# Optimization experiments

Measured on AMD Instinct MI355X. Metric: run time of the kernel, lower is better.

## Reference

```python
import jax, jax.numpy as jnp
import numpy as np

EPS = 1e-5
K = 31  # large depthwise kernel
PAD = K // 2


def _bn(x, gamma, beta, mean, var):
    # x: [B, C, L]; params: [C]
    inv = gamma / jnp.sqrt(var + EPS)
    return x * inv[:, None] + (beta - mean * inv)[:, None]


def setup_inputs() -> dict:
    key = jax.random.key(0)
    ks = jax.random.split(key, 20)
    B, C, L = 32, 256, 4096
    H = 512  # hidden = C * expand_ratio(2)

    def bn_params(k, ch):
        k1, k2, k3, k4 = jax.random.split(k, 4)
        return (jax.random.normal(k1, (ch,)) * 0.1 + 1.0,   # gamma
                jax.random.normal(k2, (ch,)) * 0.1,          # beta
                jax.random.normal(k3, (ch,)) * 0.1,          # running mean
                jax.random.uniform(k4, (ch,)) * 0.5 + 0.5)   # running var

    g0, b0, m0, v0 = bn_params(ks[0], C)
    g1, b1, m1, v1 = bn_params(ks[1], H)
    g2, b2, m2, v2 = bn_params(ks[2], H)
    g3, b3, m3, v3 = bn_params(ks[3], C)

    return {
        "x": jax.random.normal(ks[4], (B, C, L), dtype=jnp.float32),
        "w_expand": jax.random.normal(ks[5], (H, C), dtype=jnp.float32) * (1.0 / np.sqrt(C)),
        "w_dw": jax.random.normal(ks[6], (H, 1, K), dtype=jnp.float32) * (1.0 / np.sqrt(K)),
        "w_project": jax.random.normal(ks[7], (C, H), dtype=jnp.float32) * (1.0 / np.sqrt(H)),
        "g0": g0, "b0": b0, "m0": m0, "v0": v0,
        "g1": g1, "b1": b1, "m1": m1, "v1": v1,
        "g2": g2, "b2": b2, "m2": m2, "v2": v2,
        "g3": g3, "b3": b3, "m3": m3, "v3": v3,
    }


def reference(x, w_expand, w_dw, w_project,
              g0, b0, m0, v0, g1, b1, m1, v1,
              g2, b2, m2, v2, g3, b3, m3, v3):
    shortcut = x
    # pre-norm BN
    h = _bn(x, g0, b0, m0, v0)
    # pw_expand: 1x1 conv (GEMM) + BN + ReLU -> [B, H, L]
    h = jnp.einsum("bcl,hc->bhl", h, w_expand)
    h = jax.nn.relu(_bn(h, g1, b1, m1, v1))
    # large-kernel depthwise conv + BN
    H = w_dw.shape[0]
    h = jax.lax.conv_general_dilated(
        h, w_dw, window_strides=(1,), padding=[(PAD, PAD)],
        dimension_numbers=("NCH", "OIH", "NCH"), feature_group_count=H)
    h = _bn(h, g2, b2, m2, v2)
    # activation then pw_project: 1x1 conv + BN -> [B, C, L]
    h = jax.nn.relu(h)
    h = jnp.einsum("bhl,ch->bcl", h, w_project)
    h = _bn(h, g3, b3, m3, v3)
    return shortcut + h  # drop_path=0 -> identity
```

## Files before the change

kernel.cpp:

```cpp
#include <hip/hip_runtime.h>
#include <hip/hip_bf16.h>

#define C_DIM 256
#define L_DIM 4096
#define H_DIM 512
#define KW    31
#define PADW  15

typedef unsigned short u16;
typedef unsigned int   u32;
typedef short bf16x8 __attribute__((ext_vector_type(8)));
typedef float f32x4  __attribute__((ext_vector_type(4)));

__device__ __forceinline__ u16 f2bf(float f) {
    u32 u = __float_as_uint(f);
    u32 r = (u + 0x7FFFu + ((u >> 16) & 1u)) >> 16;
    return (u16)r;
}
__device__ __forceinline__ float bf2f(u16 h) {
    return __uint_as_float(((u32)h) << 16);
}

typedef __attribute__((address_space(1))) const unsigned int gq_t;
typedef __attribute__((address_space(3))) unsigned int lq_t;
__device__ __forceinline__ void async16(void* lds, const void* g) {
    __builtin_amdgcn_global_load_lds((gq_t*)g, (lq_t*)lds, 16, 0, 0);
}

__global__ __launch_bounds__(256) void prep_kernel(
    const float* __restrict__ w_expand,
    const float* __restrict__ g0, const float* __restrict__ b0,
    const float* __restrict__ m0, const float* __restrict__ v0,
    const float* __restrict__ g1, const float* __restrict__ b1,
    const float* __restrict__ m1, const float* __restrict__ v1,
    const float* __restrict__ g2, const float* __restrict__ b2,
    const float* __restrict__ m2, const float* __restrict__ v2,
    const float* __restrict__ g3, const float* __restrict__ b3,
    const float* __restrict__ m3, const float* __restrict__ v3,
    u16* __restrict__ W0bf, float* __restrict__ A1, float* __restrict__ B1,
    float* __restrict__ A2, float* __restrict__ B2,
    float* __restrict__ A3, float* __restrict__ B3)
{
    __shared__ float red[256];
    const int h = blockIdx.x;
    const int c = threadIdx.x;

    float inv0 = g0[c] / sqrtf(v0[c] + 1e-5f);
    float add0 = b0[c] - m0[c] * inv0;
    float w = w_expand[h * C_DIM + c];
    W0bf[h * C_DIM + c] = f2bf(w * inv0);
    red[c] = add0 * w;
    __syncthreads();
    for (int s = 128; s > 0; s >>= 1) {
        if (c < s) red[c] += red[c + s];
        __syncthreads();
    }
    if (c == 0) {
        float bias0 = red[0];
        float inv1 = g1[h] / sqrtf(v1[h] + 1e-5f);
        A1[h] = inv1;
        B1[h] = bias0 * inv1 + (b1[h] - m1[h] * inv1);
        float inv2 = g2[h] / sqrtf(v2[h] + 1e-5f);
        A2[h] = inv2;
        B2[h] = b2[h] - m2[h] * inv2;
        if (h < C_DIM) {
            float inv3 = g3[h] / sqrtf(v3[h] + 1e-5f);
            A3[h] = inv3;
            B3[h] = b3[h] - m3[h] * inv3;
        }
    }
}

__global__ __launch_bounds__(256) void convw_kernel(
    const float* __restrict__ w, u16* __restrict__ o, int n)
{
    int i = blockIdx.x * 256 + threadIdx.x;
    if (i < n) o[i] = f2bf(w[i]);
}

__global__ __launch_bounds__(64) void prep2_kernel(
    const float* __restrict__ w_dw, u16* __restrict__ tab)
{
    const int h = blockIdx.x;
    const int lane = threadIdx.x;
    const int l15 = lane & 15, kg = lane >> 4;
    u16* dA = tab + ((size_t)h * 64 + lane) * 8;
    u16* dB = tab + (size_t)H_DIM * 64 * 8 + ((size_t)h * 64 + lane) * 8;
#pragma unroll
    for (int j = 0; j < 8; ++j) {
        int m1 = kg * 8 + j - l15 - 1;
        int m2 = m1 + 32;
        dA[j] = (m1 >= 0 && m1 < KW) ? f2bf(w_dw[h * KW + m1]) : (u16)0;
        dB[j] = (m2 >= 0 && m2 < KW) ? f2bf(w_dw[h * KW + m2]) : (u16)0;
    }
}

__global__ __launch_bounds__(256) void convx_kernel(
    const float* __restrict__ x, u16* __restrict__ xT)
{
    __shared__ u16 t_s[64][68];
    const int b = blockIdx.z, c0 = blockIdx.y * 64, l0 = blockIdx.x * 64;
    const int tid = threadIdx.x;
    const float* xb = x + (size_t)b * C_DIM * L_DIM;
    {
        const int cl = tid >> 2, lg = (tid & 3) * 16;
        const float* src = xb + (size_t)(c0 + cl) * L_DIM + l0 + lg;
#pragma unroll
        for (int j = 0; j < 16; j += 4) {
            float4 v = *(const float4*)(src + j);
            ushort4 o;
            o.x = f2bf(v.x); o.y = f2bf(v.y); o.z = f2bf(v.z); o.w = f2bf(v.w);
            *(ushort4*)&t_s[cl][lg + j] = o;
        }
    }
    __syncthreads();
    {
        const int ll = tid >> 2, cg = (tid & 3) * 16;
        u32 w0[4], w1[4];
#pragma unroll
        for (int j = 0; j < 4; ++j) {
            w0[j] = (u32)t_s[cg + 2*j][ll] | ((u32)t_s[cg + 2*j + 1][ll] << 16);
            w1[j] = (u32)t_s[cg + 8 + 2*j][ll] | ((u32)t_s[cg + 9 + 2*j][ll] << 16);
        }
        u16* dst = xT + ((size_t)b * L_DIM + l0 + ll) * C_DIM + c0 + cg;
        uint4 o0; o0.x = w0[0]; o0.y = w0[1]; o0.z = w0[2]; o0.w = w0[3];
        uint4 o1; o1.x = w1[0]; o1.y = w1[1]; o1.z = w1[2]; o1.w = w1[3];
        *(uint4*)(dst)     = o0;
        *(uint4*)(dst + 8) = o1;
    }
}

template<int KDIM, int EPI>
__global__ __launch_bounds__(256) void gemm_bt_kernel(
    const u16* __restrict__ A,
    const u16* __restrict__ BT,
    void* __restrict__ Out,
    const float* __restrict__ Sa, const float* __restrict__ Sb,
    const float* __restrict__ Xs)
{
    __shared__ short SH[2 * 128 * 64];
    short* Asm = SH;
    short* Bsm = SH + 128 * 64;
    const int b = blockIdx.z;
    const int bm = blockIdx.y * 128;
    const int bn = blockIdx.x * 128;
    const int tid = threadIdx.x;
    const int wave = tid >> 6, lane = tid & 63;
    const int wr = wave >> 1, wc = wave & 1;
    const int l15 = lane & 15, kg = lane >> 4;

    const u16* Bb = BT + (size_t)b * L_DIM * KDIM;

    const int srow = wave * 32 + (lane >> 3);
    const int scolb = ((lane & 7) * 16) ^ ((srow & 7) << 4);
    const u16* gA = A  + (size_t)(bm + srow) * KDIM + (scolb >> 1);
    const u16* gB = Bb + (size_t)(bn + srow) * KDIM + (scolb >> 1);
    short* lA = Asm + wave * 32 * 64;
    short* lB = Bsm + wave * 32 * 64;

    const int rswz = (l15 & 7) << 4;

    f32x4 acc[4][4] = {};

    for (int kt = 0; kt < KDIM / 64; ++kt) {
        __syncthreads();
#pragma unroll
        for (int j = 0; j < 4; ++j) {
            async16(lA + j * 8 * 64, gA + (size_t)j * 8 * KDIM);
            async16(lB + j * 8 * 64, gB + (size_t)j * 8 * KDIM);
        }
        gA += 64; gB += 64;
        __syncthreads();
#pragma unroll
        for (int ks = 0; ks < 2; ++ks) {
            bf16x8 af[4], bf[4];
#pragma unroll
            for (int m = 0; m < 4; ++m)
                af[m] = *(const bf16x8*)((const char*)&Asm[(wr * 64 + m * 16 + l15) * 64]
                                         + (((ks * 64 + kg * 16)) ^ rswz));
#pragma unroll
            for (int n = 0; n < 4; ++n)
                bf[n] = *(const bf16x8*)((const char*)&Bsm[(wc * 64 + n * 16 + l15) * 64]
                                         + (((ks * 64 + kg * 16)) ^ rswz));
#pragma unroll
            for (int m = 0; m < 4; ++m)
#pragma unroll
                for (int n = 0; n < 4; ++n)
                    acc[m][n] = __builtin_amdgcn_mfma_f32_16x16x32_bf16(
                        af[m], bf[n], acc[m][n], 0, 0, 0);
        }
    }

    if constexpr (EPI == 0) {
        __syncthreads();
        char* osm = (char*)SH;
#pragma unroll
        for (int m = 0; m < 4; ++m)
#pragma unroll
        for (int r = 0; r < 4; ++r) {
            const int row = wr * 64 + m * 16 + kg * 4 + r;
            const int grow = bm + row;
            const float s = Sa[grow], t = Sb[grow];
            const int sw = (row & 7) << 4;
#pragma unroll
            for (int n = 0; n < 4; ++n) {
                const int col = wc * 64 + n * 16 + l15;
                float v = acc[m][n][r] * s + t;
                v = v > 0.f ? v : 0.f;
                *(u16*)(osm + row * 256 + ((col * 2) ^ sw)) = f2bf(v);
            }
        }
        __syncthreads();
        const int row = tid >> 1, cb0 = (tid & 1) * 128;
        const int sw = (row & 7) << 4;
        u16* dst = (u16*)Out + (size_t)b * H_DIM * L_DIM
                 + (size_t)(bm + row) * L_DIM + bn + (tid & 1) * 64;
#pragma unroll
        for (int q = 0; q < 8; ++q) {
            uint4 v = *(const uint4*)(osm + row * 256 + ((cb0 + q * 16) ^ sw));
            *(uint4*)(dst + q * 8) = v;
        }
    } else {
        float* O = (float*)Out + (size_t)b * C_DIM * L_DIM;
        const float* X = Xs + (size_t)b * C_DIM * L_DIM;
        char* osm = (char*)SH;
#pragma unroll
        for (int pass = 0; pass < 2; ++pass) {
            __syncthreads();
            if (wr == pass) {
#pragma unroll
                for (int m = 0; m < 4; ++m)
#pragma unroll
                for (int r = 0; r < 4; ++r) {
                    const int rl = m * 16 + kg * 4 + r;
                    const int grow = bm + pass * 64 + rl;
                    const float s = Sa[grow], t = Sb[grow];
                    const int sw = ((rl >> 2) & 3) << 6;
#pragma unroll
                    for (int n = 0; n < 4; ++n) {
                        const int col = wc * 64 + n * 16 + l15;
                        *(float*)(osm + rl * 512 + ((col * 4) ^ sw)) =
                            acc[m][n][r] * s + t;
                    }
                }
            }
            __syncthreads();
            const int rl = tid >> 2, c0 = (tid & 3) * 32;
            const int grow = bm + pass * 64 + rl;
            const int sw = ((rl >> 2) & 3) << 6;
            float* dst = O + (size_t)grow * L_DIM + bn + c0;
            const float* xs = X + (size_t)grow * L_DIM + bn + c0;
#pragma unroll
            for (int q = 0; q < 8; ++q) {
                float4 v = *(const float4*)(osm + rl * 512 + (((c0 + q * 4) * 4) ^ sw));
                float4 xv = *(const float4*)(xs + q * 4);
                v.x += xv.x; v.y += xv.y; v.z += xv.z; v.w += xv.w;
                *(float4*)(dst + q * 4) = v;
            }
        }
    }
}

__global__ __launch_bounds__(256) void dw_kernel(
    const u16* __restrict__ h1, const u16* __restrict__ tab,
    u16* __restrict__ h2T,
    const float* __restrict__ A2, const float* __restrict__ B2)
{
    __shared__ u16 in_s[32][320];
    __shared__ u16 out_s[256][34];
    const int b = blockIdx.z, h0 = blockIdx.y * 32, l0 = blockIdx.x * 256;
    const int tid = threadIdx.x;
    const int wave = tid >> 6, lane = tid & 63;
    const int l15 = lane & 15, kg = lane >> 4;
    const u16* hb = h1 + (size_t)b * H_DIM * L_DIM;

#pragma unroll
    for (int it = 0; it < 5; ++it) {
        const int idx = tid + it * 256;
        const int r = idx / 40, g = idx % 40;
        const int bl = l0 - 16 + g * 8;
        const u16* src = hb + (size_t)(h0 + r) * L_DIM + bl;
        uint4 val;
        if (bl >= 0 && bl + 8 <= L_DIM) {
            val = *(const uint4*)src;
        } else {
            u16 t[8];
#pragma unroll
            for (int e = 0; e < 8; ++e)
                t[e] = (bl + e >= 0 && bl + e < L_DIM) ? src[e] : (u16)0;
            val.x = (u32)t[0] | ((u32)t[1] << 16);
            val.y = (u32)t[2] | ((u32)t[3] << 16);
            val.z = (u32)t[4] | ((u32)t[5] << 16);
            val.w = (u32)t[6] | ((u32)t[7] << 16);
        }
        *(uint4*)&in_s[r][g * 8] = val;
    }
    __syncthreads();

    const u16* tabB = tab + (size_t)H_DIM * 64 * 8;
    const int xoff = 16 * l15 + 8 * kg;
#pragma unroll
    for (int hp = 0; hp < 4; ++hp) {
        const int hlA = wave * 8 + hp * 2;
        const int hA = h0 + hlA, hB = hA + 1;
        bf16x8 a1A = *(const bf16x8*)(tab  + ((size_t)hA * 64 + lane) * 8);
        bf16x8 a2A = *(const bf16x8*)(tabB + ((size_t)hA * 64 + lane) * 8);
        bf16x8 a1B = *(const bf16x8*)(tab  + ((size_t)hB * 64 + lane) * 8);
        bf16x8 a2B = *(const bf16x8*)(tabB + ((size_t)hB * 64 + lane) * 8);
        bf16x8 x1A = *(const bf16x8*)&in_s[hlA][xoff];
        bf16x8 x2A = *(const bf16x8*)&in_s[hlA][xoff + 32];
        bf16x8 x1B = *(const bf16x8*)&in_s[hlA + 1][xoff];
        bf16x8 x2B = *(const bf16x8*)&in_s[hlA + 1][xoff + 32];
        f32x4 accA = {}, accB = {};
        accA = __builtin_amdgcn_mfma_f32_16x16x32_bf16(a1A, x1A, accA, 0, 0, 0);
        accA = __builtin_amdgcn_mfma_f32_16x16x32_bf16(a2A, x2A, accA, 0, 0, 0);
        accB = __builtin_amdgcn_mfma_f32_16x16x32_bf16(a1B, x1B, accB, 0, 0, 0);
        accB = __builtin_amdgcn_mfma_f32_16x16x32_bf16(a2B, x2B, accB, 0, 0, 0);
        const float sA = A2[hA], tA = B2[hA];
        const float sB = A2[hB], tB = B2[hB];
        const int c = wave * 4 + hp;
        const int lbase = 16 * l15 + 4 * kg;
#pragma unroll
        for (int r = 0; r < 4; ++r) {
            float vA = accA[r] * sA + tA; vA = vA > 0.f ? vA : 0.f;
            float vB = accB[r] * sB + tB; vB = vB > 0.f ? vB : 0.f;
            u32 pk;
            asm("v_cvt_pk_bf16_f32 %0, %1, %2" : "=v"(pk) : "v"(vA), "v"(vB));
            const int X = lbase + r;
            const int cp = c ^ ((X >> 4) & 3);
            *(u32*)&out_s[X][cp * 2] = pk;
        }
    }
    __syncthreads();

    u32 vals[16];
#pragma unroll
    for (int c = 0; c < 16; ++c) {
        const int cp = c ^ ((tid >> 4) & 3);
        vals[c] = *(const u32*)&out_s[tid][cp * 2];
    }
    u16* dst = h2T + ((size_t)b * L_DIM + l0 + tid) * H_DIM + h0;
#pragma unroll
    for (int q = 0; q < 4; ++q) {
        uint4 o;
        o.x = vals[q * 4 + 0]; o.y = vals[q * 4 + 1];
        o.z = vals[q * 4 + 2]; o.w = vals[q * 4 + 3];
        ((uint4*)dst)[q] = o;
    }
}

extern "C" void kernel_launch(void* const* d_in, const int* in_sizes, int n_in,
                              void* d_out, int out_size, void* d_ws, size_t ws_size,
                              hipStream_t stream) {
    const float* x        = (const float*)d_in[0];
    const float* w_expand = (const float*)d_in[1];
    const float* w_dw     = (const float*)d_in[2];
    const float* w_proj   = (const float*)d_in[3];
    const float* g0 = (const float*)d_in[4],  *b0 = (const float*)d_in[5];
    const float* m0 = (const float*)d_in[6],  *v0 = (const float*)d_in[7];
    const float* g1 = (const float*)d_in[8],  *b1 = (const float*)d_in[9];
    const float* m1 = (const float*)d_in[10], *v1 = (const float*)d_in[11];
    const float* g2 = (const float*)d_in[12], *b2 = (const float*)d_in[13];
    const float* m2 = (const float*)d_in[14], *v2 = (const float*)d_in[15];
    const float* g3 = (const float*)d_in[16], *b3 = (const float*)d_in[17];
    const float* m3 = (const float*)d_in[18], *v3 = (const float*)d_in[19];
    float* out = (float*)d_out;

    const int B = in_sizes[0] / (C_DIM * L_DIM);

    char* base = (char*)d_ws;
    size_t off = 0;
    u16* W0bf = (u16*)(base + off); off += (size_t)H_DIM * C_DIM * 2;
    u16* Wpbf = (u16*)(base + off); off += (size_t)C_DIM * H_DIM * 2;
    u16* tab  = (u16*)(base + off); off += (size_t)2 * H_DIM * 64 * 8 * 2;
    float* A1p = (float*)(base + off); off += H_DIM * 4;
    float* B1p = (float*)(base + off); off += H_DIM * 4;
    float* A2p = (float*)(base + off); off += H_DIM * 4;
    float* B2p = (float*)(base + off); off += H_DIM * 4;
    float* A3p = (float*)(base + off); off += C_DIM * 4;
    float* B3p = (float*)(base + off); off += C_DIM * 4;
    off = (off + 255) & ~(size_t)255;

    const size_t per_b = ((size_t)L_DIM * C_DIM + 2 * (size_t)H_DIM * L_DIM) * 2;
    int nb = 1;
    const int cands[6] = {32, 16, 8, 4, 2, 1};
    for (int i = 0; i < 6; ++i) {
        if (B % cands[i]) continue;
        if (off + per_b * cands[i] <= ws_size) { nb = cands[i]; break; }
    }
    u16* xT  = (u16*)(base + off);
    u16* h1  = xT + (size_t)nb * L_DIM * C_DIM;
    u16* h2T = h1 + (size_t)nb * H_DIM * L_DIM;

    prep_kernel<<<H_DIM, 256, 0, stream>>>(
        w_expand, g0, b0, m0, v0, g1, b1, m1, v1, g2, b2, m2, v2,
        g3, b3, m3, v3, W0bf, A1p, B1p, A2p, B2p, A3p, B3p);
    convw_kernel<<<(C_DIM * H_DIM + 255) / 256, 256, 0, stream>>>(
        w_proj, Wpbf, C_DIM * H_DIM);
    prep2_kernel<<<H_DIM, 64, 0, stream>>>(w_dw, tab);

    for (int cs = 0; cs < B; cs += nb) {
        const float* xb = x + (size_t)cs * C_DIM * L_DIM;
        float* ob = out + (size_t)cs * C_DIM * L_DIM;
        convx_kernel<<<dim3(L_DIM / 64, C_DIM / 64, nb), 256, 0, stream>>>(xb, xT);
        gemm_bt_kernel<C_DIM, 0><<<dim3(L_DIM / 128, H_DIM / 128, nb), 256, 0, stream>>>(
            W0bf, xT, h1, A1p, B1p, nullptr);
        dw_kernel<<<dim3(L_DIM / 256, H_DIM / 32, nb), 256, 0, stream>>>(
            h1, tab, h2T, A2p, B2p);
        gemm_bt_kernel<H_DIM, 1><<<dim3(L_DIM / 128, C_DIM / 128, nb), 256, 0, stream>>>(
            Wpbf, h2T, ob, A3p, B3p, xb);
    }
}
```

Measured before the change: 343.1 us.

## Fuse depthwise conv into projection GEMM, dropping h2T intermediate buffer

Replaces the separate depthwise-conv kernel and projection GEMM with one kernel. Each block computes the depthwise conv plus BN/ReLU for 32-channel hidden chunks into LDS, then immediately feeds it as the B operand of the projection MFMA, and finally applies BN3 and the residual add. This removes the global write and read of the transposed hidden activation and one launch. In exchange, the depthwise conv is recomputed for each of the two output-channel tiles, h1 is read twice, and the kernel carries a large accumulator that may limit occupancy.

```diff
diff --git a/kernel.cpp b/kernel.cpp
--- a/kernel.cpp
+++ b/kernel.cpp
@@ -10,6 +10,7 @@
 typedef unsigned short u16;
 typedef unsigned int   u32;
 typedef short bf16x8 __attribute__((ext_vector_type(8)));
+typedef short bf16x4 __attribute__((ext_vector_type(4)));
 typedef float f32x4  __attribute__((ext_vector_type(4)));
 
 __device__ __forceinline__ u16 f2bf(float f) {
@@ -130,13 +131,12 @@
     }
 }
 
-template<int KDIM, int EPI>
+template<int KDIM>
 __global__ __launch_bounds__(256) void gemm_bt_kernel(
     const u16* __restrict__ A,
     const u16* __restrict__ BT,
-    void* __restrict__ Out,
-    const float* __restrict__ Sa, const float* __restrict__ Sb,
-    const float* __restrict__ Xs)
+    u16* __restrict__ Out,
+    const float* __restrict__ Sa, const float* __restrict__ Sb)
 {
     __shared__ short SH[2 * 128 * 64];
     short* Asm = SH;
@@ -191,161 +191,183 @@
         }
     }
 
-    if constexpr (EPI == 0) {
-        __syncthreads();
-        char* osm = (char*)SH;
+    __syncthreads();
+    char* osm = (char*)SH;
+#pragma unroll
+    for (int m = 0; m < 4; ++m)
+#pragma unroll
+    for (int r = 0; r < 4; ++r) {
+        const int row = wr * 64 + m * 16 + kg * 4 + r;
+        const int grow = bm + row;
+        const float s = Sa[grow], t = Sb[grow];
+        const int sw = (row & 7) << 4;
+#pragma unroll
+        for (int n = 0; n < 4; ++n) {
+            const int col = wc * 64 + n * 16 + l15;
+            float v = acc[m][n][r] * s + t;
+            v = v > 0.f ? v : 0.f;
+            *(u16*)(osm + row * 256 + ((col * 2) ^ sw)) = f2bf(v);
+        }
+    }
+    __syncthreads();
+    const int row = tid >> 1, cb0 = (tid & 1) * 128;
+    const int sw = (row & 7) << 4;
+    u16* dst = Out + (size_t)b * H_DIM * L_DIM
+             + (size_t)(bm + row) * L_DIM + bn + (tid & 1) * 64;
+#pragma unroll
+    for (int q = 0; q < 8; ++q) {
+        uint4 v = *(const uint4*)(osm + row * 256 + ((cb0 + q * 16) ^ sw));
+        *(uint4*)(dst + q * 8) = v;
+    }
+}
+
+__global__ __launch_bounds__(256, 2) void dwproj_kernel(
+    const u16* __restrict__ h1, const u16* __restrict__ tab,
+    const u16* __restrict__ Wp,
+    const float* __restrict__ x, float* __restrict__ out,
+    const float* __restrict__ A2, const float* __restrict__ B2,
+    const float* __restrict__ A3, const float* __restrict__ B3)
+{
+    __shared__ char SH[49152];
+    u16 (*in_s)[320] = (u16(*)[320])SH;
+    u16 (*a_s)[40]   = (u16(*)[40])(SH + 20480);
+    u32 (*o_s)[18]   = (u32(*)[18])(SH + 30720);
+
+    const int b = blockIdx.z, c0 = blockIdx.y * 128, l0 = blockIdx.x * 256;
+    const int tid = threadIdx.x;
+    const int wave = tid >> 6, lane = tid & 63;
+    const int l15 = lane & 15, kg = lane >> 4;
+    const int wr = wave >> 1, wc = wave & 1;
+
+    const u16* hb = h1 + (size_t)b * H_DIM * L_DIM;
+    const u16* tabB = tab + (size_t)H_DIM * 64 * 8;
+
+    f32x4 acc[4][8] = {};
+
+    const int ar = tid >> 1, acs = (tid & 1) * 16;
+    const int xoff = 16 * l15 + 8 * kg;
+
+    for (int hc = 0; hc < 16; ++hc) {
+        const int h0 = hc * 32;
+        __syncthreads();
+#pragma unroll
+        for (int it = 0; it < 5; ++it) {
+            const int idx = tid + it * 256;
+            const int r = idx / 40, g = idx % 40;
+            const int bl = l0 - 16 + g * 8;
+            const u16* src = hb + (size_t)(h0 + r) * L_DIM + bl;
+            uint4 val;
+            if (bl >= 0 && bl + 8 <= L_DIM) {
+                val = *(const uint4*)src;
+            } else {
+                u16 t[8];
+#pragma unroll
+                for (int e = 0; e < 8; ++e)
+                    t[e] = (bl + e >= 0 && bl + e < L_DIM) ? src[e] : (u16)0;
+                val.x = (u32)t[0] | ((u32)t[1] << 16);
+                val.y = (u32)t[2] | ((u32)t[3] << 16);
+                val.z = (u32)t[4] | ((u32)t[5] << 16);
+                val.w = (u32)t[6] | ((u32)t[7] << 16);
+            }
+            *(uint4*)&in_s[r][g * 8] = val;
+        }
+        {
+            const u16* ws = Wp + (size_t)(c0 + ar) * H_DIM + h0 + acs;
+            uint4 w0 = *(const uint4*)ws;
+            uint4 w1 = *(const uint4*)(ws + 8);
+            *(uint4*)&a_s[ar][acs] = w0;
+            *(uint4*)&a_s[ar][acs + 8] = w1;
+        }
+        __syncthreads();
+
+#pragma unroll
+        for (int hp = 0; hp < 4; ++hp) {
+            const int hl = wave * 8 + hp * 2;
+            const int ghA = h0 + hl, ghB = ghA + 1;
+            bf16x8 a1A = *(const bf16x8*)(tab  + ((size_t)ghA * 64 + lane) * 8);
+            bf16x8 a2A = *(const bf16x8*)(tabB + ((size_t)ghA * 64 + lane) * 8);
+            bf16x8 a1B = *(const bf16x8*)(tab  + ((size_t)ghB * 64 + lane) * 8);
+            bf16x8 a2B = *(const bf16x8*)(tabB + ((size_t)ghB * 64 + lane) * 8);
+            bf16x8 x1A = *(const bf16x8*)&in_s[hl][xoff];
+            bf16x8 x2A = *(const bf16x8*)&in_s[hl][xoff + 32];
+            bf16x8 x1B = *(const bf16x8*)&in_s[hl + 1][xoff];
+            bf16x8 x2B = *(const bf16x8*)&in_s[hl + 1][xoff + 32];
+            f32x4 accA = {}, accB = {};
+            accA = __builtin_amdgcn_mfma_f32_16x16x32_bf16(a1A, x1A, accA, 0, 0, 0);
+            accA = __builtin_amdgcn_mfma_f32_16x16x32_bf16(a2A, x2A, accA, 0, 0, 0);
+            accB = __builtin_amdgcn_mfma_f32_16x16x32_bf16(a1B, x1B, accB, 0, 0, 0);
+            accB = __builtin_amdgcn_mfma_f32_16x16x32_bf16(a2B, x2B, accB, 0, 0, 0);
+            const float sA = A2[ghA], tA = B2[ghA];
+            const float sB = A2[ghB], tB = B2[ghB];
+            const int pair = wave * 4 + hp;
+            const int col8 = pair >> 1;
+            const int lbase = 16 * l15 + 4 * kg;
+#pragma unroll
+            for (int r = 0; r < 4; ++r) {
+                float vA = accA[r] * sA + tA; vA = vA > 0.f ? vA : 0.f;
+                float vB = accB[r] * sB + tB; vB = vB > 0.f ? vB : 0.f;
+                u32 pk;
+                asm("v_cvt_pk_bf16_f32 %0, %1, %2" : "=v"(pk) : "v"(vA), "v"(vB));
+                const int X = lbase + r;
+                const int sw = (X >> 1) & 7;
+                o_s[X][(col8 ^ sw) * 2 + (pair & 1)] = pk;
+            }
+        }
+        __syncthreads();
+
+        bf16x8 af[4];
 #pragma unroll
         for (int m = 0; m < 4; ++m)
-#pragma unroll
-        for (int r = 0; r < 4; ++r) {
-            const int row = wr * 64 + m * 16 + kg * 4 + r;
-            const int grow = bm + row;
-            const float s = Sa[grow], t = Sb[grow];
-            const int sw = (row & 7) << 4;
-#pragma unroll
-            for (int n = 0; n < 4; ++n) {
-                const int col = wc * 64 + n * 16 + l15;
-                float v = acc[m][n][r] * s + t;
-                v = v > 0.f ? v : 0.f;
-                *(u16*)(osm + row * 256 + ((col * 2) ^ sw)) = f2bf(v);
-            }
-        }
-        __syncthreads();
-        const int row = tid >> 1, cb0 = (tid & 1) * 128;
-        const int sw = (row & 7) << 4;
-        u16* dst = (u16*)Out + (size_t)b * H_DIM * L_DIM
-                 + (size_t)(bm + row) * L_DIM + bn + (tid & 1) * 64;
-#pragma unroll
-        for (int q = 0; q < 8; ++q) {
-            uint4 v = *(const uint4*)(osm + row * 256 + ((cb0 + q * 16) ^ sw));
-            *(uint4*)(dst + q * 8) = v;
-        }
-    } else {
-        float* O = (float*)Out + (size_t)b * C_DIM * L_DIM;
-        const float* X = Xs + (size_t)b * C_DIM * L_DIM;
-        char* osm = (char*)SH;
-#pragma unroll
-        for (int pass = 0; pass < 2; ++pass) {
-            __syncthreads();
-            if (wr == pass) {
-#pragma unroll
-                for (int m = 0; m < 4; ++m)
+            af[m] = *(const bf16x8*)&a_s[wr * 64 + m * 16 + l15][kg * 8];
+#pragma unroll
+        for (int n = 0; n < 8; ++n) {
+            const int l = wc * 128 + n * 16 + l15;
+            const int sw = (l >> 1) & 7;
+            bf16x4 blo = *(const bf16x4*)&o_s[l][((2 * kg) ^ sw) * 2];
+            bf16x4 bhi = *(const bf16x4*)&o_s[l][((2 * kg + 1) ^ sw) * 2];
+            bf16x8 bf = __builtin_shufflevector(blo, bhi, 0, 1, 2, 3, 4, 5, 6, 7);
+#pragma unroll
+            for (int m = 0; m < 4; ++m)
+                acc[m][n] = __builtin_amdgcn_mfma_f32_16x16x32_bf16(
+                    af[m], bf, acc[m][n], 0, 0, 0);
+        }
+    }
+
+    float* ep = (float*)SH;
+    const float* xb = x + (size_t)b * C_DIM * L_DIM;
+    float* ob = out + (size_t)b * C_DIM * L_DIM;
+#pragma unroll
+    for (int p = 0; p < 4; ++p) {
+        __syncthreads();
+        if (wr == (p >> 1)) {
+#pragma unroll
+            for (int mm = 0; mm < 2; ++mm) {
+                const int m = (p & 1) * 2 + mm;
 #pragma unroll
                 for (int r = 0; r < 4; ++r) {
-                    const int rl = m * 16 + kg * 4 + r;
-                    const int grow = bm + pass * 64 + rl;
-                    const float s = Sa[grow], t = Sb[grow];
-                    const int sw = ((rl >> 2) & 3) << 6;
-#pragma unroll
-                    for (int n = 0; n < 4; ++n) {
-                        const int col = wc * 64 + n * 16 + l15;
-                        *(float*)(osm + rl * 512 + ((col * 4) ^ sw)) =
-                            acc[m][n][r] * s + t;
+                    const int rl = mm * 16 + kg * 4 + r;
+                    const int grow = c0 + p * 32 + rl;
+                    const float s3 = A3[grow], t3 = B3[grow];
+#pragma unroll
+                    for (int n = 0; n < 8; ++n) {
+                        const int col = wc * 128 + n * 16 + l15;
+                        ep[rl * 260 + col] = acc[m][n][r] * s3 + t3;
                     }
                 }
             }
-            __syncthreads();
-            const int rl = tid >> 2, c0 = (tid & 3) * 32;
-            const int grow = bm + pass * 64 + rl;
-            const int sw = ((rl >> 2) & 3) << 6;
-            float* dst = O + (size_t)grow * L_DIM + bn + c0;
-            const float* xs = X + (size_t)grow * L_DIM + bn + c0;
-#pragma unroll
-            for (int q = 0; q < 8; ++q) {
-                float4 v = *(const float4*)(osm + rl * 512 + (((c0 + q * 4) * 4) ^ sw));
-                float4 xv = *(const float4*)(xs + q * 4);
-                v.x += xv.x; v.y += xv.y; v.z += xv.z; v.w += xv.w;
-                *(float4*)(dst + q * 4) = v;
-            }
-        }
-    }
-}
-
-__global__ __launch_bounds__(256) void dw_kernel(
-    const u16* __restrict__ h1, const u16* __restrict__ tab,
-    u16* __restrict__ h2T,
-    const float* __restrict__ A2, const float* __restrict__ B2)
-{
-    __shared__ u16 in_s[32][320];
-    __shared__ u16 out_s[256][34];
-    const int b = blockIdx.z, h0 = blockIdx.y * 32, l0 = blockIdx.x * 256;
-    const int tid = threadIdx.x;
-    const int wave = tid >> 6, lane = tid & 63;
-    const int l15 = lane & 15, kg = lane >> 4;
-    const u16* hb = h1 + (size_t)b * H_DIM * L_DIM;
-
-#pragma unroll
-    for (int it = 0; it < 5; ++it) {
-        const int idx = tid + it * 256;
-        const int r = idx / 40, g = idx % 40;
-        const int bl = l0 - 16 + g * 8;
-        const u16* src = hb + (size_t)(h0 + r) * L_DIM + bl;
-        uint4 val;
-        if (bl >= 0 && bl + 8 <= L_DIM) {
-            val = *(const uint4*)src;
-        } else {
-            u16 t[8];
-#pragma unroll
-            for (int e = 0; e < 8; ++e)
-                t[e] = (bl + e >= 0 && bl + e < L_DIM) ? src[e] : (u16)0;
-            val.x = (u32)t[0] | ((u32)t[1] << 16);
-            val.y = (u32)t[2] | ((u32)t[3] << 16);
-            val.z = (u32)t[4] | ((u32)t[5] << 16);
-            val.w = (u32)t[6] | ((u32)t[7] << 16);
-        }
-        *(uint4*)&in_s[r][g * 8] = val;
-    }
-    __syncthreads();
-
-    const u16* tabB = tab + (size_t)H_DIM * 64 * 8;
-    const int xoff = 16 * l15 + 8 * kg;
-#pragma unroll
-    for (int hp = 0; hp < 4; ++hp) {
-        const int hlA = wave * 8 + hp * 2;
-        const int hA = h0 + hlA, hB = hA + 1;
-        bf16x8 a1A = *(const bf16x8*)(tab  + ((size_t)hA * 64 + lane) * 8);
-        bf16x8 a2A = *(const bf16x8*)(tabB + ((size_t)hA * 64 + lane) * 8);
-        bf16x8 a1B = *(const bf16x8*)(tab  + ((size_t)hB * 64 + lane) * 8);
-        bf16x8 a2B = *(const bf16x8*)(tabB + ((size_t)hB * 64 + lane) * 8);
-        bf16x8 x1A = *(const bf16x8*)&in_s[hlA][xoff];
-        bf16x8 x2A = *(const bf16x8*)&in_s[hlA][xoff + 32];
-        bf16x8 x1B = *(const bf16x8*)&in_s[hlA + 1][xoff];
-        bf16x8 x2B = *(const bf16x8*)&in_s[hlA + 1][xoff + 32];
-        f32x4 accA = {}, accB = {};
-        accA = __builtin_amdgcn_mfma_f32_16x16x32_bf16(a1A, x1A, accA, 0, 0, 0);
-        accA = __builtin_amdgcn_mfma_f32_16x16x32_bf16(a2A, x2A, accA, 0, 0, 0);
-        accB = __builtin_amdgcn_mfma_f32_16x16x32_bf16(a1B, x1B, accB, 0, 0, 0);
-        accB = __builtin_amdgcn_mfma_f32_16x16x32_bf16(a2B, x2B, accB, 0, 0, 0);
-        const float sA = A2[hA], tA = B2[hA];
-        const float sB = A2[hB], tB = B2[hB];
-        const int c = wave * 4 + hp;
-        const int lbase = 16 * l15 + 4 * kg;
-#pragma unroll
-        for (int r = 0; r < 4; ++r) {
-            float vA = accA[r] * sA + tA; vA = vA > 0.f ? vA : 0.f;
-            float vB = accB[r] * sB + tB; vB = vB > 0.f ? vB : 0.f;
-            u32 pk;
-            asm("v_cvt_pk_bf16_f32 %0, %1, %2" : "=v"(pk) : "v"(vA), "v"(vB));
-            const int X = lbase + r;
-            const int cp = c ^ ((X >> 4) & 3);
-            *(u32*)&out_s[X][cp * 2] = pk;
-        }
-    }
-    __syncthreads();
-
-    u32 vals[16];
-#pragma unroll
-    for (int c = 0; c < 16; ++c) {
-        const int cp = c ^ ((tid >> 4) & 3);
-        vals[c] = *(const u32*)&out_s[tid][cp * 2];
-    }
-    u16* dst = h2T + ((size_t)b * L_DIM + l0 + tid) * H_DIM + h0;
-#pragma unroll
-    for (int q = 0; q < 4; ++q) {
-        uint4 o;
-        o.x = vals[q * 4 + 0]; o.y = vals[q * 4 + 1];
-        o.z = vals[q * 4 + 2]; o.w = vals[q * 4 + 3];
-        ((uint4*)dst)[q] = o;
+        }
+        __syncthreads();
+        const int rowp = tid >> 3, lseg = (tid & 7) * 32;
+        const int grow = c0 + p * 32 + rowp;
+        float* dst = ob + (size_t)grow * L_DIM + l0 + lseg;
+        const float* xs = xb + (size_t)grow * L_DIM + l0 + lseg;
+#pragma unroll
+        for (int q = 0; q < 8; ++q) {
+            float4 v = *(const float4*)&ep[rowp * 260 + lseg + q * 4];
+            float4 xv = *(const float4*)(xs + q * 4);
+            v.x += xv.x; v.y += xv.y; v.z += xv.z; v.w += xv.w;
+            *(float4*)(dst + q * 4) = v;
+        }
     }
 }
 
@@ -381,7 +403,7 @@
     float* B3p = (float*)(base + off); off += C_DIM * 4;
     off = (off + 255) & ~(size_t)255;
 
-    const size_t per_b = ((size_t)L_DIM * C_DIM + 2 * (size_t)H_DIM * L_DIM) * 2;
+    const size_t per_b = ((size_t)L_DIM * C_DIM + (size_t)H_DIM * L_DIM) * 2;
     int nb = 1;
     const int cands[6] = {32, 16, 8, 4, 2, 1};
     for (int i = 0; i < 6; ++i) {
@@ -390,7 +412,6 @@
     }
     u16* xT  = (u16*)(base + off);
     u16* h1  = xT + (size_t)nb * L_DIM * C_DIM;
-    u16* h2T = h1 + (size_t)nb * H_DIM * L_DIM;
 
     prep_kernel<<<H_DIM, 256, 0, stream>>>(
         w_expand, g0, b0, m0, v0, g1, b1, m1, v1, g2, b2, m2, v2,
@@ -403,11 +424,9 @@
         const float* xb = x + (size_t)cs * C_DIM * L_DIM;
         float* ob = out + (size_t)cs * C_DIM * L_DIM;
         convx_kernel<<<dim3(L_DIM / 64, C_DIM / 64, nb), 256, 0, stream>>>(xb, xT);
-        gemm_bt_kernel<C_DIM, 0><<<dim3(L_DIM / 128, H_DIM / 128, nb), 256, 0, stream>>>(
-            W0bf, xT, h1, A1p, B1p, nullptr);
-        dw_kernel<<<dim3(L_DIM / 256, H_DIM / 32, nb), 256, 0, stream>>>(
-            h1, tab, h2T, A2p, B2p);
-        gemm_bt_kernel<H_DIM, 1><<<dim3(L_DIM / 128, C_DIM / 128, nb), 256, 0, stream>>>(
-            Wpbf, h2T, ob, A3p, B3p, xb);
-    }
-}
+        gemm_bt_kernel<C_DIM><<<dim3(L_DIM / 128, H_DIM / 128, nb), 256, 0, stream>>>(
+            W0bf, xT, h1, A1p, B1p);
+        dwproj_kernel<<<dim3(L_DIM / 256, C_DIM / 128, nb), 256, 0, stream>>>(
+            h1, tab, Wpbf, xb, ob, A2p, B2p, A3p, B3p);
+    }
+}
```

New measurement: 412.6 us. +20.3%, slower.
